# Kernel tuning notes

Measured on AMD Instinct MI355X. Metric: run time of the kernel, lower is better.

## Reference

```python
import jax, jax.numpy as jnp
import numpy as np

EPS = 1e-8  # torch.nn.CosineSimilarity default eps
VOCAB, D = 100000, 300
S, A, W = 256, 256, 8


def setup_inputs() -> dict:
    key = jax.random.key(0)
    k1, k2, k3 = jax.random.split(key, 3)
    emb = jax.random.normal(k1, (VOCAB, D), dtype=jnp.float32)
    sen_cats = jax.random.randint(k2, (S, W), 0, VOCAB, dtype=jnp.int64)
    ann_cats = jax.random.randint(k3, (A, W), 0, VOCAB, dtype=jnp.int64)
    return {"emb": emb, "sen_cats": sen_cats, "ann_cats": ann_cats, "none_idx": 0}


def _forward(emb, sen_cats, ann_cats, none_idx):
    sen_e = emb[sen_cats]            # [S, W, D] per-word embeddings (get_cat_emb)
    ann_e = emb[ann_cats]            # [A, W, D]
    none_emb = emb[none_idx]         # [D]

    # cosine similarity for every (sen word, ann word) pair: [S, A, W, W]
    dots = jnp.einsum('swd,avd->sawv', sen_e, ann_e)
    ns = jnp.linalg.norm(sen_e, axis=-1)   # [S, W]
    na = jnp.linalg.norm(ann_e, axis=-1)   # [A, W]
    denom = jnp.maximum(ns[:, None, :, None] * na[None, :, None, :], EPS)
    cos = dots / denom

    # sen word equal to none embedding -> sim forced to 0 (torch.equal branch)
    sen_none = jnp.all(sen_e == none_emb, axis=-1)             # [S, W]
    sim = jnp.where(sen_none[:, None, :, None], jnp.zeros((), cos.dtype), cos)

    # faithful order-dependent running update: start 0;
    # max_sim = sim if (sim >= max_sim or sim < 0); sen word is outer loop.
    n_pairs = sim.shape[2] * sim.shape[3]
    sims_seq = sim.reshape(sim.shape[0], sim.shape[1], n_pairs).transpose(2, 0, 1)  # [W*W, S, A]

    def step(cur, s):
        new = jnp.where((s >= cur) | (s < 0), s, cur)
        return new, None

    max_sim, _ = jax.lax.scan(step, jnp.zeros(sim.shape[:2], sim.dtype), sims_seq)  # [S, A]

    sen_wd_emb = sen_e.sum(axis=1)  # [S, D] (stack(...).sum(0) per sen category)
    return max_sim, sen_wd_emb


def reference(emb, sen_cats, ann_cats, none_idx):
    return _forward(emb, sen_cats, ann_cats, none_idx)
```

## Files before the change

kernel.cpp:

```cpp
#include <hip/hip_runtime.h>
#include <hip/hip_fp16.h>

#define D 300
#define NS 256
#define NA 256
#define W 8
#define NPH 5

typedef _Float16 half8 __attribute__((ext_vector_type(8)));
typedef float f32x4 __attribute__((ext_vector_type(4)));

__global__ __launch_bounds__(256, 1) void k_all(const float* __restrict__ emb,
                                                const int* __restrict__ sen_cats,
                                                const int* __restrict__ ann_cats,
                                                const int* __restrict__ none_idx,
                                                float* __restrict__ out) {
    __shared__ float smem[16384];
    _Float16* stage = reinterpret_cast<_Float16*>(smem);
    float* rsc = smem + 8192;
    _Float16* cosld = reinterpret_cast<_Float16*>(smem);

    int tid = threadIdx.x;
    int blk = blockIdx.x;
    int by = blk >> 4, bx = blk & 15;
    int wv = tid >> 6, lane = tid & 63;
    int wy = wv >> 1, wx = wv & 1;
    int lr = lane & 15, lk = lane >> 4;

    int g = tid >> 4, f0 = tid & 15;
    int c0 = f0 >> 3, lk0 = (f0 & 7) >> 1, e0 = (f0 & 1) * 4;
    const float* rowp[16];
    int catA[8];
#pragma unroll
    for (int j = 0; j < 8; ++j) {
        catA[j] = sen_cats[by * 128 + g + j * 16];
        rowp[j] = emb + (size_t)catA[j] * D;
    }
#pragma unroll
    for (int j = 8; j < 16; ++j) {
        int cb = ann_cats[bx * 128 + g + (j - 8) * 16];
        rowp[j] = emb + (size_t)cb * D;
    }

    float4 pf[16];
    float na[16];
#pragma unroll
    for (int j = 0; j < 16; ++j) na[j] = 0.f;

#define PH_LOAD(p)                                                            \
    {                                                                         \
        int gk = (p) * 64 + f0 * 4;                                           \
        bool ok = ((p) < 4) || (f0 <= 10);          \
        _Pragma("unroll")                                                     \
        for (int j = 0; j < 16; ++j)                                          \
            pf[j] = ok ? *reinterpret_cast<const float4*>(rowp[j] + gk)       \
                       : make_float4(0.f, 0.f, 0.f, 0.f);                     \
    }
#define PH_WRITE(b)                                                           \
    {                                                                         \
        _Pragma("unroll")                                                     \
        for (int j = 0; j < 16; ++j) {                                        \
            float4 v = pf[j];                                                 \
            na[j] = fmaf(v.x, v.x, na[j]); na[j] = fmaf(v.y, v.y, na[j]);     \
            na[j] = fmaf(v.z, v.z, na[j]); na[j] = fmaf(v.w, v.w, na[j]);     \
            ushort4 h;                                                        \
            h.x = __half_as_ushort(__float2half(v.x));                        \
            h.y = __half_as_ushort(__float2half(v.y));                        \
            h.z = __half_as_ushort(__float2half(v.z));                        \
            h.w = __half_as_ushort(__float2half(v.w));                        \
            int rt = (j < 8) ? j : (j - 8);                                   \
            int off = (b) * 16384 + ((j < 8) ? 0 : 8192) +                    \
                      ((rt * 2 + c0) * 64 + lk0 * 16 + g) * 8 + e0;           \
            *reinterpret_cast<ushort4*>(stage + off) = h;                     \
        }                                                                     \
    }

    f32x4 acc[4][4] = {};

    PH_LOAD(0);
    PH_WRITE(0);
    PH_LOAD(1);
    __syncthreads();

#pragma unroll
    for (int p = 0; p < NPH; ++p) {
        if (p + 1 < NPH) {
            PH_WRITE((p + 1) & 1);
            if (p + 2 < NPH) PH_LOAD(p + 2);
        }
        int bb = (p & 1) * 16384;
#pragma unroll
        for (int c = 0; c < 2; ++c) {
            half8 Ah[4], Bh[4];
#pragma unroll
            for (int m = 0; m < 4; ++m)
                Ah[m] = *reinterpret_cast<const half8*>(
                    stage + bb + (((wy * 4 + m) * 2 + c) * 64 + lane) * 8);
#pragma unroll
            for (int n = 0; n < 4; ++n)
                Bh[n] = *reinterpret_cast<const half8*>(
                    stage + bb + 8192 + (((wx * 4 + n) * 2 + c) * 64 + lane) * 8);
#pragma unroll
            for (int m = 0; m < 4; ++m)
#pragma unroll
                for (int n = 0; n < 4; ++n)
                    acc[m][n] = __builtin_amdgcn_mfma_f32_16x16x32_f16(
                        Ah[m], Bh[n], acc[m][n], 0, 0, 0);
        }
        __syncthreads();
    }

    int nidx = none_idx[0];
#pragma unroll
    for (int j = 0; j < 16; ++j) {
        float s = na[j];
        s += __shfl_xor(s, 1, 64);
        s += __shfl_xor(s, 2, 64);
        s += __shfl_xor(s, 4, 64);
        s += __shfl_xor(s, 8, 64);
        if (f0 == 0) {
            float rn = (float)(1.0 / sqrt((double)s));
            if (j < 8 && catA[j] == nidx) rn = 0.f;
            rsc[g + ((j < 8) ? j * 16 : 128 + (j - 8) * 16)] = rn;
        }
    }
    __syncthreads();

#pragma unroll
    for (int m = 0; m < 4; ++m) {
        int rbase = wy * 64 + m * 16 + lk * 4;
#pragma unroll
        for (int r = 0; r < 4; ++r) {
            float sA = rsc[rbase + r];
#pragma unroll
            for (int n = 0; n < 4; ++n) {
                int lc = wx * 64 + n * 16 + lr;
                float sB = rsc[128 + lc];
                cosld[(rbase + r) * 128 + lc] = (_Float16)(acc[m][n][r] * sA * sB);
            }
        }
    }
    __syncthreads();

    int pi = tid >> 4, pj = tid & 15;
    float cur = 0.f;
#pragma unroll
    for (int w = 0; w < W; ++w) {
        const _Float16* rp = &cosld[(pi * 8 + w) * 128 + pj * 8];
#pragma unroll
        for (int v = 0; v < W; ++v) {
            float sv = (float)rp[v];
            cur = (sv >= cur || sv < 0.f) ? sv : cur;
        }
    }
    out[(by * 16 + pi) * NA + (bx * 16 + pj)] = cur;

    if (wv == 0) {
        int cb = blk;
        float4 s0 = make_float4(0.f, 0.f, 0.f, 0.f);
        float4 s1 = make_float4(0.f, 0.f, 0.f, 0.f);
#pragma unroll
        for (int w = 0; w < W; ++w) {
            int cat = sen_cats[cb * W + w];
            const float4* src = reinterpret_cast<const float4*>(emb + (size_t)cat * D);
            float4 v0 = src[lane];
            s0.x += v0.x; s0.y += v0.y; s0.z += v0.z; s0.w += v0.w;
            if (lane < 11) {
                float4 v1 = src[lane + 64];
                s1.x += v1.x; s1.y += v1.y; s1.z += v1.z; s1.w += v1.w;
            }
        }
        float4* o = reinterpret_cast<float4*>(out + NS * NA + (size_t)cb * D);
        o[lane] = s0;
        if (lane < 11) o[lane + 64] = s1;
    }
#undef PH_LOAD
#undef PH_WRITE
}

extern "C" void kernel_launch(void* const* d_in, const int* in_sizes, int n_in,
                              void* d_out, int out_size, void* d_ws, size_t ws_size,
                              hipStream_t stream) {
    const float* emb = (const float*)d_in[0];
    const int* sen = (const int*)d_in[1];
    const int* ann = (const int*)d_in[2];
    const int* none = (const int*)d_in[3];
    float* out = (float*)d_out;

    hipLaunchKernelGGL(k_all, dim3(256), dim3(256), 0, stream,
                       emb, sen, ann, none, out);
}
```

Measured before the change: 23.54 us.

## Split block into producer and consumer wavefronts for gather and MFMA overlap

Doubles the block to 512 threads. Four producer waves gather embedding rows, convert them to fp16 into double-buffered LDS, compute the inverse norms, and write the sentence-embedding sums. Four consumer waves run the MFMA matmul, the scaling, and the running-max scan. The goal is to overlap global gather latency with tensor-core work, at the cost of more threads and a fragile barrier count that must match across both roles. The producers also load each phase right before writing it, so there is less prefetch depth per thread.

```diff
diff --git a/kernel.cpp b/kernel.cpp
--- a/kernel.cpp
+++ b/kernel.cpp
@@ -10,7 +10,7 @@
 typedef _Float16 half8 __attribute__((ext_vector_type(8)));
 typedef float f32x4 __attribute__((ext_vector_type(4)));
 
-__global__ __launch_bounds__(256, 1) void k_all(const float* __restrict__ emb,
+__global__ __launch_bounds__(512, 1) void k_all(const float* __restrict__ emb,
                                                 const int* __restrict__ sen_cats,
                                                 const int* __restrict__ ann_cats,
                                                 const int* __restrict__ none_idx,
@@ -24,33 +24,34 @@
     int blk = blockIdx.x;
     int by = blk >> 4, bx = blk & 15;
     int wv = tid >> 6, lane = tid & 63;
-    int wy = wv >> 1, wx = wv & 1;
-    int lr = lane & 15, lk = lane >> 4;
+    bool producer = (wv >= 4);
 
-    int g = tid >> 4, f0 = tid & 15;
-    int c0 = f0 >> 3, lk0 = (f0 & 7) >> 1, e0 = (f0 & 1) * 4;
-    const float* rowp[16];
-    int catA[8];
+    if (producer) {
+        int ptid = tid - 256;
+        int g = ptid >> 4, f0 = ptid & 15;
+        int c0 = f0 >> 3, lk0 = (f0 & 7) >> 1, e0 = (f0 & 1) * 4;
+        const float* rowp[16];
+        int catA[8];
 #pragma unroll
-    for (int j = 0; j < 8; ++j) {
-        catA[j] = sen_cats[by * 128 + g + j * 16];
-        rowp[j] = emb + (size_t)catA[j] * D;
-    }
+        for (int j = 0; j < 8; ++j) {
+            catA[j] = sen_cats[by * 128 + g + j * 16];
+            rowp[j] = emb + (size_t)catA[j] * D;
+        }
 #pragma unroll
-    for (int j = 8; j < 16; ++j) {
-        int cb = ann_cats[bx * 128 + g + (j - 8) * 16];
-        rowp[j] = emb + (size_t)cb * D;
-    }
+        for (int j = 8; j < 16; ++j) {
+            int cb = ann_cats[bx * 128 + g + (j - 8) * 16];
+            rowp[j] = emb + (size_t)cb * D;
+        }
 
-    float4 pf[16];
-    float na[16];
+        float4 pf[16];
+        float na[16];
 #pragma unroll
-    for (int j = 0; j < 16; ++j) na[j] = 0.f;
+        for (int j = 0; j < 16; ++j) na[j] = 0.f;
 
 #define PH_LOAD(p)                                                            \
     {                                                                         \
         int gk = (p) * 64 + f0 * 4;                                           \
-        bool ok = ((p) < 4) || (f0 <= 10);          \
+        bool ok = ((p) < 4) || (f0 <= 10);                                    \
         _Pragma("unroll")                                                     \
         for (int j = 0; j < 16; ++j)                                          \
             pf[j] = ok ? *reinterpret_cast<const float4*>(rowp[j] + gk)       \
@@ -75,107 +76,107 @@
         }                                                                     \
     }
 
-    f32x4 acc[4][4] = {};
-
-    PH_LOAD(0);
-    PH_WRITE(0);
-    PH_LOAD(1);
-    __syncthreads();
+        PH_LOAD(0);
+        PH_WRITE(0);
+        __syncthreads();
 
 #pragma unroll
-    for (int p = 0; p < NPH; ++p) {
-        if (p + 1 < NPH) {
-            PH_WRITE((p + 1) & 1);
-            if (p + 2 < NPH) PH_LOAD(p + 2);
+        for (int p = 0; p < NPH; ++p) {
+            if (p + 1 < NPH) {
+                PH_LOAD(p + 1);
+                PH_WRITE((p + 1) & 1);
+            } else {
+                int nidx = none_idx[0];
+#pragma unroll
+                for (int j = 0; j < 16; ++j) {
+                    float s = na[j];
+                    s += __shfl_xor(s, 1, 64);
+                    s += __shfl_xor(s, 2, 64);
+                    s += __shfl_xor(s, 4, 64);
+                    s += __shfl_xor(s, 8, 64);
+                    if (f0 == 0) {
+                        float rn = (float)(1.0 / sqrt((double)s));
+                        if (j < 8 && catA[j] == nidx) rn = 0.f;
+                        rsc[g + ((j < 8) ? j * 16 : 128 + (j - 8) * 16)] = rn;
+                    }
+                }
+            }
+            __syncthreads();
         }
-        int bb = (p & 1) * 16384;
+
+        if (ptid < 75) {
+            float4 s = make_float4(0.f, 0.f, 0.f, 0.f);
 #pragma unroll
-        for (int c = 0; c < 2; ++c) {
-            half8 Ah[4], Bh[4];
+            for (int w = 0; w < W; ++w) {
+                int cat = sen_cats[blk * W + w];
+                float4 v = reinterpret_cast<const float4*>(emb + (size_t)cat * D)[ptid];
+                s.x += v.x; s.y += v.y; s.z += v.z; s.w += v.w;
+            }
+            reinterpret_cast<float4*>(out + NS * NA + (size_t)blk * D)[ptid] = s;
+        }
+        __syncthreads();
+#undef PH_LOAD
+#undef PH_WRITE
+    } else {
+        int wy = wv >> 1, wx = wv & 1;
+        int lr = lane & 15, lk = lane >> 4;
+
+        f32x4 acc[4][4] = {};
+        __syncthreads();
+
 #pragma unroll
-            for (int m = 0; m < 4; ++m)
-                Ah[m] = *reinterpret_cast<const half8*>(
-                    stage + bb + (((wy * 4 + m) * 2 + c) * 64 + lane) * 8);
+        for (int p = 0; p < NPH; ++p) {
+            int bb = (p & 1) * 16384;
 #pragma unroll
-            for (int n = 0; n < 4; ++n)
-                Bh[n] = *reinterpret_cast<const half8*>(
-                    stage + bb + 8192 + (((wx * 4 + n) * 2 + c) * 64 + lane) * 8);
+            for (int c = 0; c < 2; ++c) {
+                half8 Ah[4], Bh[4];
 #pragma unroll
-            for (int m = 0; m < 4; ++m)
+                for (int m = 0; m < 4; ++m)
+                    Ah[m] = *reinterpret_cast<const half8*>(
+                        stage + bb + (((wy * 4 + m) * 2 + c) * 64 + lane) * 8);
 #pragma unroll
                 for (int n = 0; n < 4; ++n)
-                    acc[m][n] = __builtin_amdgcn_mfma_f32_16x16x32_f16(
-                        Ah[m], Bh[n], acc[m][n], 0, 0, 0);
+                    Bh[n] = *reinterpret_cast<const half8*>(
+                        stage + bb + 8192 + (((wx * 4 + n) * 2 + c) * 64 + lane) * 8);
+#pragma unroll
+                for (int m = 0; m < 4; ++m)
+#pragma unroll
+                    for (int n = 0; n < 4; ++n)
+                        acc[m][n] = __builtin_amdgcn_mfma_f32_16x16x32_f16(
+                            Ah[m], Bh[n], acc[m][n], 0, 0, 0);
+            }
+            __syncthreads();
+        }
+
+#pragma unroll
+        for (int m = 0; m < 4; ++m) {
+            int rbase = wy * 64 + m * 16 + lk * 4;
+#pragma unroll
+            for (int r = 0; r < 4; ++r) {
+                float sA = rsc[rbase + r];
+#pragma unroll
+                for (int n = 0; n < 4; ++n) {
+                    int lc = wx * 64 + n * 16 + lr;
+                    float sB = rsc[128 + lc];
+                    cosld[(rbase + r) * 128 + lc] = (_Float16)(acc[m][n][r] * sA * sB);
+                }
+            }
         }
         __syncthreads();
-    }
 
-    int nidx = none_idx[0];
+        int pi = tid >> 4, pj = tid & 15;
+        float cur = 0.f;
 #pragma unroll
-    for (int j = 0; j < 16; ++j) {
-        float s = na[j];
-        s += __shfl_xor(s, 1, 64);
-        s += __shfl_xor(s, 2, 64);
-        s += __shfl_xor(s, 4, 64);
-        s += __shfl_xor(s, 8, 64);
-        if (f0 == 0) {
-            float rn = (float)(1.0 / sqrt((double)s));
-            if (j < 8 && catA[j] == nidx) rn = 0.f;
-            rsc[g + ((j < 8) ? j * 16 : 128 + (j - 8) * 16)] = rn;
-        }
-    }
-    __syncthreads();
-
+        for (int w = 0; w < W; ++w) {
+            const _Float16* rp = &cosld[(pi * 8 + w) * 128 + pj * 8];
 #pragma unroll
-    for (int m = 0; m < 4; ++m) {
-        int rbase = wy * 64 + m * 16 + lk * 4;
-#pragma unroll
-        for (int r = 0; r < 4; ++r) {
-            float sA = rsc[rbase + r];
-#pragma unroll
-            for (int n = 0; n < 4; ++n) {
-                int lc = wx * 64 + n * 16 + lr;
-                float sB = rsc[128 + lc];
-                cosld[(rbase + r) * 128 + lc] = (_Float16)(acc[m][n][r] * sA * sB);
+            for (int v = 0; v < W; ++v) {
+                float sv = (float)rp[v];
+                cur = (sv >= cur || sv < 0.f) ? sv : cur;
             }
         }
+        out[(by * 16 + pi) * NA + (bx * 16 + pj)] = cur;
     }
-    __syncthreads();
-
-    int pi = tid >> 4, pj = tid & 15;
-    float cur = 0.f;
-#pragma unroll
-    for (int w = 0; w < W; ++w) {
-        const _Float16* rp = &cosld[(pi * 8 + w) * 128 + pj * 8];
-#pragma unroll
-        for (int v = 0; v < W; ++v) {
-            float sv = (float)rp[v];
-            cur = (sv >= cur || sv < 0.f) ? sv : cur;
-        }
-    }
-    out[(by * 16 + pi) * NA + (bx * 16 + pj)] = cur;
-
-    if (wv == 0) {
-        int cb = blk;
-        float4 s0 = make_float4(0.f, 0.f, 0.f, 0.f);
-        float4 s1 = make_float4(0.f, 0.f, 0.f, 0.f);
-#pragma unroll
-        for (int w = 0; w < W; ++w) {
-            int cat = sen_cats[cb * W + w];
-            const float4* src = reinterpret_cast<const float4*>(emb + (size_t)cat * D);
-            float4 v0 = src[lane];
-            s0.x += v0.x; s0.y += v0.y; s0.z += v0.z; s0.w += v0.w;
-            if (lane < 11) {
-                float4 v1 = src[lane + 64];
-                s1.x += v1.x; s1.y += v1.y; s1.z += v1.z; s1.w += v1.w;
-            }
-        }
-        float4* o = reinterpret_cast<float4*>(out + NS * NA + (size_t)cb * D);
-        o[lane] = s0;
-        if (lane < 11) o[lane + 64] = s1;
-    }
-#undef PH_LOAD
-#undef PH_WRITE
 }
 
 extern "C" void kernel_launch(void* const* d_in, const int* in_sizes, int n_in,
@@ -187,6 +188,6 @@
     const int* none = (const int*)d_in[3];
     float* out = (float*)d_out;
 
-    hipLaunchKernelGGL(k_all, dim3(256), dim3(256), 0, stream,
+    hipLaunchKernelGGL(k_all, dim3(256), dim3(512), 0, stream,
                        emb, sen, ann, none, out);
 }
```

Result: slower. 31.31 us (+33.0%).
